# Optimization experiments

Hardware: AMD Instinct MI355X
Metric: run time of the kernel (lower is better)

## Reference

```python
import jax, jax.numpy as jnp
import numpy as np

B, T, D, H = 32, 512, 512, 1024


def setup_inputs() -> dict:
    key = jax.random.key(0)
    k1, k2, k3 = jax.random.split(key, 3)
    X = jax.random.normal(k1, (B, T, D), dtype=jnp.float32)
    # TF GRUCell variables: gates/kernel [D+H, 2H], gates/bias [2H] (init 1.0),
    # candidate/kernel [D+H, H], candidate/bias [H] (init 0.0). Use small random
    # values for a non-degenerate numerical baseline.
    gate_kernel = jax.random.normal(k2, (D + H, 2 * H), dtype=jnp.float32) * 0.02
    gate_bias = jnp.ones((2 * H,), dtype=jnp.float32)
    cand_kernel = jax.random.normal(k3, (D + H, H), dtype=jnp.float32) * 0.02
    cand_bias = jnp.zeros((H,), dtype=jnp.float32)
    return {"X": X, "gate_kernel": gate_kernel, "gate_bias": gate_bias,
            "cand_kernel": cand_kernel, "cand_bias": cand_bias}


def reference(X, gate_kernel, gate_bias, cand_kernel, cand_bias):
    """Static unidirectional GRU (TF GRUCell math), activation=tanh.
    Returns stacked per-step hidden states [B, T, H]; final state is out[:, -1]."""
    h0 = jnp.zeros((X.shape[0], cand_kernel.shape[1]), dtype=X.dtype)

    def step(h, x_t):
        # gates: r (reset), u (update) = sigmoid([x, h] @ Wg + bg)
        gates = jax.nn.sigmoid(jnp.concatenate([x_t, h], axis=-1) @ gate_kernel + gate_bias)
        r, u = jnp.split(gates, 2, axis=-1)
        # candidate: tanh([x, r*h] @ Wc + bc)
        c = jnp.tanh(jnp.concatenate([x_t, r * h], axis=-1) @ cand_kernel + cand_bias)
        h_new = u * h + (1.0 - u) * c
        return h_new, h_new

    _, hs = jax.lax.scan(step, h0, jnp.swapaxes(X, 0, 1))  # hs: [T, B, H]
    return jnp.swapaxes(hs, 0, 1)  # [B, T, H]
```

## Files before the change

kernel.cpp:

```cpp
#include <hip/hip_runtime.h>
#include <hip/hip_bf16.h>

typedef short s8v __attribute__((ext_vector_type(8)));
typedef float f4v __attribute__((ext_vector_type(4)));
typedef unsigned int u4v __attribute__((ext_vector_type(4)));
typedef unsigned int u2v __attribute__((ext_vector_type(2)));

#define NBLK 64
#define TPB 512

constexpr int BB = 32, TT = 512, DD = 512, HH = 1024;
constexpr int KK = DD + HH;
constexpr int PK = KK + 8;
constexpr int PK8 = PK / 8;
constexpr int K8 = KK / 8;

constexpr size_t OFF_WGT = 0;
constexpr size_t SZ_WGT  = (size_t)2 * HH * KK * 2;
constexpr size_t OFF_WCT = OFF_WGT + SZ_WGT;
constexpr size_t SZ_WCT  = (size_t)HH * KK * 2;
constexpr size_t OFF_XBF = OFF_WCT + SZ_WCT;
constexpr size_t SZ_XBF  = (size_t)BB * TT * DD * 2;
constexpr size_t OFF_HPB = OFF_XBF + SZ_XBF;
constexpr size_t SZ_PUB  = (size_t)BB * HH * 2;
constexpr size_t OFF_RPB = OFF_HPB + SZ_PUB;
constexpr size_t OFF_FLG = OFF_RPB + SZ_PUB;
constexpr size_t SZ_FLG  = (size_t)2 * NBLK * 2 * 16 * 4;

__global__ void wtr_kernel(const float* __restrict__ in, unsigned short* __restrict__ out, int N) {
    __shared__ float tl[32][33];
    int tx = threadIdx.x & 31, ty = threadIdx.x >> 5;
    int n0 = blockIdx.x * 32, k0 = blockIdx.y * 32;
#pragma unroll
    for (int r = ty; r < 32; r += 8) tl[r][tx] = in[(size_t)(k0 + r) * N + n0 + tx];
    __syncthreads();
#pragma unroll
    for (int r = ty; r < 32; r += 8) {
        __hip_bfloat16 h = __float2bfloat16(tl[tx][r]);
        out[(size_t)(n0 + r) * KK + k0 + tx] = *reinterpret_cast<unsigned short*>(&h);
    }
}

__global__ void xconv_kernel(const float* __restrict__ X, unsigned short* __restrict__ Xbf) {
    size_t i = ((size_t)blockIdx.x * 256 + threadIdx.x) * 4;
    float4 v = *reinterpret_cast<const float4*>(X + i);
    __hip_bfloat16 h0 = __float2bfloat16(v.x), h1 = __float2bfloat16(v.y);
    __hip_bfloat16 h2 = __float2bfloat16(v.z), h3 = __float2bfloat16(v.w);
    ushort4 o;
    o.x = *(unsigned short*)&h0; o.y = *(unsigned short*)&h1;
    o.z = *(unsigned short*)&h2; o.w = *(unsigned short*)&h3;
    *reinterpret_cast<ushort4*>(Xbf + i) = o;
}

__device__ __forceinline__ u4v cload16(const void* p) {
    u4v r; asm volatile("global_load_dwordx4 %0, %1, off sc0 sc1" : "=v"(r) : "v"(p) : "memory"); return r;
}
__device__ __forceinline__ void cstore8(void* p, u2v v) {
    asm volatile("global_store_dwordx2 %0, %1, off sc0 sc1" :: "v"(p), "v"(v) : "memory");
}
#define B16(x) __builtin_bit_cast(s8v, (x))
#define WAIT_VM(n) do { asm volatile("s_waitcnt vmcnt(" #n ")" ::: "memory"); \
                        __builtin_amdgcn_sched_barrier(0); } while (0)

__device__ __forceinline__ void poll16(const int* f, int blk0, int rtw, int gen, int lane) {
    if (lane < 16) {
        const int* fp = f + ((size_t)(blk0 + lane) * 2 + rtw) * 16;
        while (__hip_atomic_load(fp, __ATOMIC_RELAXED, __HIP_MEMORY_SCOPE_AGENT) < gen)
            __builtin_amdgcn_s_sleep(1);
    }
    asm volatile("" ::: "memory");
}

#define MFMA(A, B, C) __builtin_amdgcn_mfma_f32_16x16x32_bf16((A), (B), (C), 0, 0, 0)

__global__ __launch_bounds__(TPB, 1) void gru_kernel(
    const unsigned short* __restrict__ Xbf,
    const unsigned short* __restrict__ WgT,
    const unsigned short* __restrict__ WcT,
    const float* __restrict__ bg,
    const float* __restrict__ bc,
    float* __restrict__ out,
    unsigned short* __restrict__ hpub,
    unsigned short* __restrict__ rpub,
    int* __restrict__ gflagA,
    int* __restrict__ gflagB)
{
    __shared__ unsigned short sWg[32 * PK];
    __shared__ unsigned short sWc[16 * PK];
    __shared__ float sP[3][2][2][16][16];
    __shared__ unsigned short sStage[32][16];

    const int b    = blockIdx.x;
    const int tid  = threadIdx.x;
    const int wid  = tid >> 6;
    const int lane = tid & 63;
    const int l15  = lane & 15;
    const int lq   = lane >> 4;
    const int ks   = wid >> 1;
    const int rt   = wid & 1;
    const int roff = rt * 16;
    const int arow = roff + l15;
    const int bcol0= b * 16;

    {
        s8v* dst = (s8v*)sWg;
        for (int idx = tid; idx < 32 * K8; idx += TPB) {
            int c = idx / K8, k8 = idx % K8;
            int gc = (c < 16) ? (bcol0 + c) : (HH + bcol0 + (c - 16));
            dst[c * PK8 + k8] = ((const s8v*)(WgT + (size_t)gc * KK))[k8];
        }
        s8v* dst2 = (s8v*)sWc;
        for (int idx = tid; idx < 16 * K8; idx += TPB) {
            int c = idx / K8, k8 = idx % K8;
            dst2[c * PK8 + k8] = ((const s8v*)(WcT + (size_t)(bcol0 + c) * KK))[k8];
        }
    }

    const float bgr = bg[bcol0 + l15];
    const float bgu = bg[HH + bcol0 + l15];
    const float bcv = bc[bcol0 + l15];
    const int   ccol = bcol0 + l15;

    const s8v* sWg8 = (const s8v*)sWg;
    const s8v* sWc8 = (const s8v*)sWc;
    const s8v* bwr = sWg8 + l15 * PK8 + lq;
    const s8v* bwu = sWg8 + (16 + l15) * PK8 + lq;
    const s8v* bwc = sWc8 + l15 * PK8 + lq;
    const s8v* bwrx = bwr + 16 * ks;
    const s8v* bwux = bwu + 16 * ks;
    const s8v* bwrh = bwr + 64 + 32 * ks;
    const s8v* bwuh = bwu + 64 + 32 * ks;
    const s8v* bwcx = bwc + 16 * ks;
    const s8v* bwch = bwc + 64 + 32 * ks;

    float hprev[4] = {0.f, 0.f, 0.f, 0.f};
    float ureg[4]  = {0.f, 0.f, 0.f, 0.f};

    __syncthreads();

#pragma unroll 1
    for (int t = 0; t < TT; ++t) {
        const s8v* xk = (const s8v*)(Xbf + (size_t)arow * (TT * DD) + (size_t)t * DD) + lq + 16 * ks;

        f4v ar0 = {0,0,0,0}, ar1 = {0,0,0,0}, au0 = {0,0,0,0}, au1 = {0,0,0,0};
        {
            s8v x0 = xk[0], x1 = xk[4], x2 = xk[8], x3 = xk[12];
            ar0 = MFMA(x0, bwrx[0],  ar0); au0 = MFMA(x0, bwux[0],  au0);
            ar1 = MFMA(x1, bwrx[4],  ar1); au1 = MFMA(x1, bwux[4],  au1);
            ar0 = MFMA(x2, bwrx[8],  ar0); au0 = MFMA(x2, bwux[8],  au0);
            ar1 = MFMA(x3, bwrx[12], ar1); au1 = MFMA(x3, bwux[12], au1);
        }

        if (t > 0) {
            poll16(gflagB, ks * 16, rt, t, lane);
            const unsigned short* hp = hpub + (size_t)arow * HH + ks * 256 + lq * 8;
            u4v hb[8];
#pragma unroll
            for (int j = 0; j < 8; ++j) hb[j] = cload16(hp + (size_t)j * 32);
            WAIT_VM(4);
            ar0 = MFMA(B16(hb[0]), bwrh[0],  ar0); au0 = MFMA(B16(hb[0]), bwuh[0],  au0);
            ar1 = MFMA(B16(hb[1]), bwrh[4],  ar1); au1 = MFMA(B16(hb[1]), bwuh[4],  au1);
            ar0 = MFMA(B16(hb[2]), bwrh[8],  ar0); au0 = MFMA(B16(hb[2]), bwuh[8],  au0);
            ar1 = MFMA(B16(hb[3]), bwrh[12], ar1); au1 = MFMA(B16(hb[3]), bwuh[12], au1);
            WAIT_VM(0);
            ar0 = MFMA(B16(hb[4]), bwrh[16], ar0); au0 = MFMA(B16(hb[4]), bwuh[16], au0);
            ar1 = MFMA(B16(hb[5]), bwrh[20], ar1); au1 = MFMA(B16(hb[5]), bwuh[20], au1);
            ar0 = MFMA(B16(hb[6]), bwrh[24], ar0); au0 = MFMA(B16(hb[6]), bwuh[24], au0);
            ar1 = MFMA(B16(hb[7]), bwrh[28], ar1); au1 = MFMA(B16(hb[7]), bwuh[28], au1);
        }

        f4v pr = ar0 + ar1, pu = au0 + au1;
        if (ks > 0) {
#pragma unroll
            for (int i = 0; i < 4; ++i) {
                sP[ks - 1][rt][0][lq * 4 + i][l15] = pr[i];
                sP[ks - 1][rt][1][lq * 4 + i][l15] = pu[i];
            }
        }
        __syncthreads();
        float zr[4], zu[4];
        if (ks == 0) {
#pragma unroll
            for (int i = 0; i < 4; ++i) {
                int rr = lq * 4 + i;
                zr[i] = pr[i] + sP[0][rt][0][rr][l15] + sP[1][rt][0][rr][l15]
                              + sP[2][rt][0][rr][l15] + bgr;
                zu[i] = pu[i] + sP[0][rt][1][rr][l15] + sP[1][rt][1][rr][l15]
                              + sP[2][rt][1][rr][l15] + bgu;
            }
        }
        __syncthreads();
        if (ks == 0) {
#pragma unroll
            for (int i = 0; i < 4; ++i) {
                float r = 1.f / (1.f + __expf(-zr[i]));
                ureg[i] = 1.f / (1.f + __expf(-zu[i]));
                __hip_bfloat16 hb16 = __float2bfloat16(r * hprev[i]);
                sStage[roff + lq * 4 + i][l15] = *(unsigned short*)&hb16;
            }
            if (t > 0) {
                int prow = roff + (lane >> 2), pc4 = (lane & 3) * 4;
                u2v v = *reinterpret_cast<const u2v*>(&sStage[prow][pc4]);
                cstore8(rpub + (size_t)prow * HH + bcol0 + pc4, v);
                asm volatile("s_waitcnt vmcnt(0)" ::: "memory");
                if (lane == 0)
                    __hip_atomic_store(&gflagA[(b * 2 + rt) * 16], t,
                                       __ATOMIC_RELAXED, __HIP_MEMORY_SCOPE_AGENT);
            }
        }

        f4v c0 = {0,0,0,0}, c1 = {0,0,0,0};
        {
            s8v x0 = xk[0], x1 = xk[4], x2 = xk[8], x3 = xk[12];
            c0 = MFMA(x0, bwcx[0],  c0); c1 = MFMA(x1, bwcx[4],  c1);
            c0 = MFMA(x2, bwcx[8],  c0); c1 = MFMA(x3, bwcx[12], c1);
        }

        if (t > 0) {
            poll16(gflagA, ks * 16, rt, t, lane);
            const unsigned short* rp = rpub + (size_t)arow * HH + ks * 256 + lq * 8;
            u4v rb[8];
#pragma unroll
            for (int j = 0; j < 8; ++j) rb[j] = cload16(rp + (size_t)j * 32);
            WAIT_VM(4);
            c0 = MFMA(B16(rb[0]), bwch[0],  c0); c1 = MFMA(B16(rb[1]), bwch[4],  c1);
            c0 = MFMA(B16(rb[2]), bwch[8],  c0); c1 = MFMA(B16(rb[3]), bwch[12], c1);
            WAIT_VM(0);
            c0 = MFMA(B16(rb[4]), bwch[16], c0); c1 = MFMA(B16(rb[5]), bwch[20], c1);
            c0 = MFMA(B16(rb[6]), bwch[24], c0); c1 = MFMA(B16(rb[7]), bwch[28], c1);
        }

        f4v pc = c0 + c1;
        if (ks > 0) {
#pragma unroll
            for (int i = 0; i < 4; ++i) sP[ks - 1][rt][0][lq * 4 + i][l15] = pc[i];
        }
        __syncthreads();
        float zc[4];
        if (ks == 0) {
#pragma unroll
            for (int i = 0; i < 4; ++i) {
                int rr = lq * 4 + i;
                zc[i] = pc[i] + sP[0][rt][0][rr][l15] + sP[1][rt][0][rr][l15]
                              + sP[2][rt][0][rr][l15] + bcv;
            }
        }
        __syncthreads();
        if (ks == 0) {
#pragma unroll
            for (int i = 0; i < 4; ++i) {
                float e = __expf(2.f * zc[i]);
                float cv = 1.f - 2.f / (e + 1.f);
                float hn = ureg[i] * hprev[i] + (1.f - ureg[i]) * cv;
                hprev[i] = hn;
                __hip_bfloat16 hb16 = __float2bfloat16(hn);
                sStage[roff + lq * 4 + i][l15] = *(unsigned short*)&hb16;
            }
            int prow = roff + (lane >> 2), pc4 = (lane & 3) * 4;
            u2v v = *reinterpret_cast<const u2v*>(&sStage[prow][pc4]);
            cstore8(hpub + (size_t)prow * HH + bcol0 + pc4, v);
            asm volatile("s_waitcnt vmcnt(0)" ::: "memory");
            if (lane == 0)
                __hip_atomic_store(&gflagB[(b * 2 + rt) * 16], t + 1,
                                   __ATOMIC_RELAXED, __HIP_MEMORY_SCOPE_AGENT);
#pragma unroll
            for (int i = 0; i < 4; ++i) {
                int row = roff + lq * 4 + i;
                out[(size_t)row * (TT * HH) + (size_t)t * HH + ccol] = hprev[i];
            }
        }
    }
}

extern "C" void kernel_launch(void* const* d_in, const int* in_sizes, int n_in,
                              void* d_out, int out_size, void* d_ws, size_t ws_size,
                              hipStream_t stream) {
    const float* X  = (const float*)d_in[0];
    const float* gk = (const float*)d_in[1];
    const float* gb = (const float*)d_in[2];
    const float* ck = (const float*)d_in[3];
    const float* cb = (const float*)d_in[4];
    float* out = (float*)d_out;
    char* ws = (char*)d_ws;
    if (ws_size < OFF_FLG + SZ_FLG) return;

    unsigned short* WgT  = (unsigned short*)(ws + OFF_WGT);
    unsigned short* WcT  = (unsigned short*)(ws + OFF_WCT);
    unsigned short* Xbf  = (unsigned short*)(ws + OFF_XBF);
    unsigned short* hpub = (unsigned short*)(ws + OFF_HPB);
    unsigned short* rpub = (unsigned short*)(ws + OFF_RPB);
    int*            gflagA = (int*)(ws + OFF_FLG);
    int*            gflagB = gflagA + NBLK * 2 * 16;

    hipMemsetAsync(gflagA, 0, SZ_FLG, stream);

    dim3 tb(256);
    wtr_kernel<<<dim3(2 * HH / 32, KK / 32), tb, 0, stream>>>(gk, WgT, 2 * HH);
    wtr_kernel<<<dim3(HH / 32, KK / 32), tb, 0, stream>>>(ck, WcT, HH);
    xconv_kernel<<<(BB * TT * DD) / (256 * 4), tb, 0, stream>>>(X, Xbf);

    gru_kernel<<<NBLK, dim3(TPB), 0, stream>>>(Xbf, WgT, WcT, gb, cb, out,
                                               hpub, rpub, gflagA, gflagB);
}
```

Baseline: 3.914 ms.

## Embed step-tag in bf16 exponent bits to validate data without flag polling

Published h and r*h values are scaled by a per-step power of two so that their bf16 exponent bits carry a step class tag. Consumers load the data speculatively, check the tag bits, and fall back to flag polling only when the data is stale. The r buffer is double-buffered, the store-then-flag wait is removed, and the x-part MFMAs are overlapped with the speculative loads. This is meant to cut the cross-block handshake latency on each step, at the cost of clamping tiny magnitudes, relying on value-range assumptions that could break correctness, and retry loops when reads arrive early.

```diff
diff --git a/kernel.cpp b/kernel.cpp
--- a/kernel.cpp
+++ b/kernel.cpp
@@ -14,6 +14,7 @@
 constexpr int PK = KK + 8;
 constexpr int PK8 = PK / 8;
 constexpr int K8 = KK / 8;
+constexpr size_t BBHH = (size_t)BB * HH;
 
 constexpr size_t OFF_WGT = 0;
 constexpr size_t SZ_WGT  = (size_t)2 * HH * KK * 2;
@@ -22,9 +23,9 @@
 constexpr size_t OFF_XBF = OFF_WCT + SZ_WCT;
 constexpr size_t SZ_XBF  = (size_t)BB * TT * DD * 2;
 constexpr size_t OFF_HPB = OFF_XBF + SZ_XBF;
-constexpr size_t SZ_PUB  = (size_t)BB * HH * 2;
+constexpr size_t SZ_PUB  = BBHH * 2;
 constexpr size_t OFF_RPB = OFF_HPB + SZ_PUB;
-constexpr size_t OFF_FLG = OFF_RPB + SZ_PUB;
+constexpr size_t OFF_FLG = OFF_RPB + 2 * SZ_PUB;
 constexpr size_t SZ_FLG  = (size_t)2 * NBLK * 2 * 16 * 4;
 
 __global__ void wtr_kernel(const float* __restrict__ in, unsigned short* __restrict__ out, int N) {
@@ -58,6 +59,9 @@
 __device__ __forceinline__ void cstore8(void* p, u2v v) {
     asm volatile("global_store_dwordx2 %0, %1, off sc0 sc1" :: "v"(p), "v"(v) : "memory");
 }
+__device__ __forceinline__ void cstore4(void* p, int v) {
+    asm volatile("global_store_dword %0, %1, off sc0 sc1" :: "v"(p), "v"(v) : "memory");
+}
 #define B16(x) __builtin_bit_cast(s8v, (x))
 #define WAIT_VM(n) do { asm volatile("s_waitcnt vmcnt(" #n ")" ::: "memory"); \
                         __builtin_amdgcn_sched_barrier(0); } while (0)
@@ -72,6 +76,26 @@
 }
 
 #define MFMA(A, B, C) __builtin_amdgcn_mfma_f32_16x16x32_bf16((A), (B), (C), 0, 0, 0)
+
+__device__ __forceinline__ float enc(float h, float s) {
+    float a = __builtin_fmaxf(__builtin_fabsf(h), 9.313225746154785e-10f);
+    return __builtin_copysignf(a, h) * s;
+}
+__device__ __forceinline__ float cls_scale(int c) {
+    return __builtin_bit_cast(float, (unsigned)(127 + 32 * c) << 23);
+}
+__device__ __forceinline__ float cls_inv(int c) {
+    return __builtin_bit_cast(float, (unsigned)(127 - 32 * c) << 23);
+}
+__device__ __forceinline__ unsigned cls_pat(int c) {
+    return 0x30003000u + (unsigned)c * 0x10001000u;
+}
+#define VALID8(arr, e, bad) do { bad = 0u; \
+    _Pragma("unroll") for (int j_ = 0; j_ < 8; ++j_) { \
+        bad |= ((arr)[j_][0] & 0x70007000u) ^ (e); \
+        bad |= ((arr)[j_][1] & 0x70007000u) ^ (e); \
+        bad |= ((arr)[j_][2] & 0x70007000u) ^ (e); \
+        bad |= ((arr)[j_][3] & 0x70007000u) ^ (e); } } while (0)
 
 __global__ __launch_bounds__(TPB, 1) void gru_kernel(
     const unsigned short* __restrict__ Xbf,
@@ -88,7 +112,7 @@
     __shared__ unsigned short sWg[32 * PK];
     __shared__ unsigned short sWc[16 * PK];
     __shared__ float sP[3][2][2][16][16];
-    __shared__ unsigned short sStage[32][16];
+    __shared__ unsigned short sStage[2][16][16];
 
     const int b    = blockIdx.x;
     const int tid  = threadIdx.x;
@@ -116,9 +140,9 @@
         }
     }
 
-    const float bgr = bg[bcol0 + l15];
-    const float bgu = bg[HH + bcol0 + l15];
-    const float bcv = bc[bcol0 + l15];
+    const float bgr  = bg[bcol0 + l15];
+    const float bgu  = bg[HH + bcol0 + l15];
+    const float bcv  = bc[bcol0 + l15];
     const int   ccol = bcol0 + l15;
 
     const s8v* sWg8 = (const s8v*)sWg;
@@ -141,35 +165,47 @@
 #pragma unroll 1
     for (int t = 0; t < TT; ++t) {
         const s8v* xk = (const s8v*)(Xbf + (size_t)arow * (TT * DD) + (size_t)t * DD) + lq + 16 * ks;
-
-        f4v ar0 = {0,0,0,0}, ar1 = {0,0,0,0}, au0 = {0,0,0,0}, au1 = {0,0,0,0};
-        {
-            s8v x0 = xk[0], x1 = xk[4], x2 = xk[8], x3 = xk[12];
-            ar0 = MFMA(x0, bwrx[0],  ar0); au0 = MFMA(x0, bwux[0],  au0);
-            ar1 = MFMA(x1, bwrx[4],  ar1); au1 = MFMA(x1, bwux[4],  au1);
-            ar0 = MFMA(x2, bwrx[8],  ar0); au0 = MFMA(x2, bwux[8],  au0);
-            ar1 = MFMA(x3, bwrx[12], ar1); au1 = MFMA(x3, bwux[12], au1);
-        }
-
+        s8v x0 = xk[0], x1 = xk[4], x2 = xk[8], x3 = xk[12];
+
+        u4v hb[8];
+        const unsigned short* hp = hpub + (size_t)arow * HH + ks * 256 + lq * 8;
         if (t > 0) {
-            poll16(gflagB, ks * 16, rt, t, lane);
-            const unsigned short* hp = hpub + (size_t)arow * HH + ks * 256 + lq * 8;
-            u4v hb[8];
 #pragma unroll
             for (int j = 0; j < 8; ++j) hb[j] = cload16(hp + (size_t)j * 32);
-            WAIT_VM(4);
-            ar0 = MFMA(B16(hb[0]), bwrh[0],  ar0); au0 = MFMA(B16(hb[0]), bwuh[0],  au0);
-            ar1 = MFMA(B16(hb[1]), bwrh[4],  ar1); au1 = MFMA(B16(hb[1]), bwuh[4],  au1);
-            ar0 = MFMA(B16(hb[2]), bwrh[8],  ar0); au0 = MFMA(B16(hb[2]), bwuh[8],  au0);
-            ar1 = MFMA(B16(hb[3]), bwrh[12], ar1); au1 = MFMA(B16(hb[3]), bwuh[12], au1);
+        }
+        f4v axr = {0,0,0,0}, axu = {0,0,0,0};
+        axr = MFMA(x0, bwrx[0],  axr); axu = MFMA(x0, bwux[0],  axu);
+        axr = MFMA(x1, bwrx[4],  axr); axu = MFMA(x1, bwux[4],  axu);
+        axr = MFMA(x2, bwrx[8],  axr); axu = MFMA(x2, bwux[8],  axu);
+        axr = MFMA(x3, bwrx[12], axr); axu = MFMA(x3, bwux[12], axu);
+
+        f4v ahr0 = {0,0,0,0}, ahr1 = {0,0,0,0}, ahu0 = {0,0,0,0}, ahu1 = {0,0,0,0};
+        if (t > 0) {
             WAIT_VM(0);
-            ar0 = MFMA(B16(hb[4]), bwrh[16], ar0); au0 = MFMA(B16(hb[4]), bwuh[16], au0);
-            ar1 = MFMA(B16(hb[5]), bwrh[20], ar1); au1 = MFMA(B16(hb[5]), bwuh[20], au1);
-            ar0 = MFMA(B16(hb[6]), bwrh[24], ar0); au0 = MFMA(B16(hb[6]), bwuh[24], au0);
-            ar1 = MFMA(B16(hb[7]), bwrh[28], ar1); au1 = MFMA(B16(hb[7]), bwuh[28], au1);
-        }
-
-        f4v pr = ar0 + ar1, pu = au0 + au1;
+            const unsigned eA = cls_pat((t - 1) & 3);
+            unsigned bad; VALID8(hb, eA, bad);
+            if (__any(bad != 0)) {
+                poll16(gflagB, ks * 16, rt, t, lane);
+                do {
+#pragma unroll
+                    for (int j = 0; j < 8; ++j) hb[j] = cload16(hp + (size_t)j * 32);
+                    WAIT_VM(0);
+                    VALID8(hb, eA, bad);
+                } while (__any(bad != 0));
+            }
+            ahr0 = MFMA(B16(hb[0]), bwrh[0],  ahr0); ahu0 = MFMA(B16(hb[0]), bwuh[0],  ahu0);
+            ahr1 = MFMA(B16(hb[1]), bwrh[4],  ahr1); ahu1 = MFMA(B16(hb[1]), bwuh[4],  ahu1);
+            ahr0 = MFMA(B16(hb[2]), bwrh[8],  ahr0); ahu0 = MFMA(B16(hb[2]), bwuh[8],  ahu0);
+            ahr1 = MFMA(B16(hb[3]), bwrh[12], ahr1); ahu1 = MFMA(B16(hb[3]), bwuh[12], ahu1);
+            ahr0 = MFMA(B16(hb[4]), bwrh[16], ahr0); ahu0 = MFMA(B16(hb[4]), bwuh[16], ahu0);
+            ahr1 = MFMA(B16(hb[5]), bwrh[20], ahr1); ahu1 = MFMA(B16(hb[5]), bwuh[20], ahu1);
+            ahr0 = MFMA(B16(hb[6]), bwrh[24], ahr0); ahu0 = MFMA(B16(hb[6]), bwuh[24], ahu0);
+            ahr1 = MFMA(B16(hb[7]), bwrh[28], ahr1); ahu1 = MFMA(B16(hb[7]), bwuh[28], ahu1);
+        }
+        const float hinv = cls_inv((t - 1) & 3);
+        f4v pr = axr + (ahr0 + ahr1) * hinv;
+        f4v pu = axu + (ahu0 + ahu1) * hinv;
+
         if (ks > 0) {
 #pragma unroll
             for (int i = 0; i < 4; ++i) {
@@ -190,47 +226,56 @@
             }
         }
         __syncthreads();
+        const float sEnc = cls_scale(t & 3);
         if (ks == 0) {
 #pragma unroll
             for (int i = 0; i < 4; ++i) {
                 float r = 1.f / (1.f + __expf(-zr[i]));
                 ureg[i] = 1.f / (1.f + __expf(-zu[i]));
-                __hip_bfloat16 hb16 = __float2bfloat16(r * hprev[i]);
-                sStage[roff + lq * 4 + i][l15] = *(unsigned short*)&hb16;
+                __hip_bfloat16 hb16 = __float2bfloat16(enc(r * hprev[i], sEnc));
+                sStage[rt][lq * 4 + i][l15] = *(unsigned short*)&hb16;
             }
             if (t > 0) {
-                int prow = roff + (lane >> 2), pc4 = (lane & 3) * 4;
-                u2v v = *reinterpret_cast<const u2v*>(&sStage[prow][pc4]);
-                cstore8(rpub + (size_t)prow * HH + bcol0 + pc4, v);
-                asm volatile("s_waitcnt vmcnt(0)" ::: "memory");
-                if (lane == 0)
-                    __hip_atomic_store(&gflagA[(b * 2 + rt) * 16], t,
-                                       __ATOMIC_RELAXED, __HIP_MEMORY_SCOPE_AGENT);
-            }
-        }
-
-        f4v c0 = {0,0,0,0}, c1 = {0,0,0,0};
-        {
-            s8v x0 = xk[0], x1 = xk[4], x2 = xk[8], x3 = xk[12];
-            c0 = MFMA(x0, bwcx[0],  c0); c1 = MFMA(x1, bwcx[4],  c1);
-            c0 = MFMA(x2, bwcx[8],  c0); c1 = MFMA(x3, bwcx[12], c1);
-        }
-
+                int prow = lane >> 2, pc4 = (lane & 3) * 4;
+                u2v v = *reinterpret_cast<const u2v*>(&sStage[rt][prow][pc4]);
+                cstore8(rpub + (size_t)(t & 1) * BBHH + (size_t)(roff + prow) * HH + bcol0 + pc4, v);
+                if (lane == 0) cstore4(gflagA + (b * 2 + rt) * 16, t);
+            }
+        }
+
+        u4v rb[8];
+        const unsigned short* rp = rpub + (size_t)(t & 1) * BBHH
+                                 + (size_t)arow * HH + ks * 256 + lq * 8;
         if (t > 0) {
-            poll16(gflagA, ks * 16, rt, t, lane);
-            const unsigned short* rp = rpub + (size_t)arow * HH + ks * 256 + lq * 8;
-            u4v rb[8];
 #pragma unroll
             for (int j = 0; j < 8; ++j) rb[j] = cload16(rp + (size_t)j * 32);
-            WAIT_VM(4);
-            c0 = MFMA(B16(rb[0]), bwch[0],  c0); c1 = MFMA(B16(rb[1]), bwch[4],  c1);
-            c0 = MFMA(B16(rb[2]), bwch[8],  c0); c1 = MFMA(B16(rb[3]), bwch[12], c1);
+        }
+        f4v cx0 = {0,0,0,0}, cx1 = {0,0,0,0};
+        cx0 = MFMA(x0, bwcx[0],  cx0); cx1 = MFMA(x1, bwcx[4],  cx1);
+        cx0 = MFMA(x2, bwcx[8],  cx0); cx1 = MFMA(x3, bwcx[12], cx1);
+
+        f4v ch0 = {0,0,0,0}, ch1 = {0,0,0,0};
+        if (t > 0) {
             WAIT_VM(0);
-            c0 = MFMA(B16(rb[4]), bwch[16], c0); c1 = MFMA(B16(rb[5]), bwch[20], c1);
-            c0 = MFMA(B16(rb[6]), bwch[24], c0); c1 = MFMA(B16(rb[7]), bwch[28], c1);
-        }
-
-        f4v pc = c0 + c1;
+            const unsigned eB = cls_pat(t & 3);
+            unsigned bad; VALID8(rb, eB, bad);
+            if (__any(bad != 0)) {
+                poll16(gflagA, ks * 16, rt, t, lane);
+                do {
+#pragma unroll
+                    for (int j = 0; j < 8; ++j) rb[j] = cload16(rp + (size_t)j * 32);
+                    WAIT_VM(0);
+                    VALID8(rb, eB, bad);
+                } while (__any(bad != 0));
+            }
+            ch0 = MFMA(B16(rb[0]), bwch[0],  ch0); ch1 = MFMA(B16(rb[1]), bwch[4],  ch1);
+            ch0 = MFMA(B16(rb[2]), bwch[8],  ch0); ch1 = MFMA(B16(rb[3]), bwch[12], ch1);
+            ch0 = MFMA(B16(rb[4]), bwch[16], ch0); ch1 = MFMA(B16(rb[5]), bwch[20], ch1);
+            ch0 = MFMA(B16(rb[6]), bwch[24], ch0); ch1 = MFMA(B16(rb[7]), bwch[28], ch1);
+        }
+        const float rinv = cls_inv(t & 3);
+        f4v pc = (cx0 + cx1) + (ch0 + ch1) * rinv;
+
         if (ks > 0) {
 #pragma unroll
             for (int i = 0; i < 4; ++i) sP[ks - 1][rt][0][lq * 4 + i][l15] = pc[i];
@@ -253,16 +298,13 @@
                 float cv = 1.f - 2.f / (e + 1.f);
                 float hn = ureg[i] * hprev[i] + (1.f - ureg[i]) * cv;
                 hprev[i] = hn;
-                __hip_bfloat16 hb16 = __float2bfloat16(hn);
-                sStage[roff + lq * 4 + i][l15] = *(unsigned short*)&hb16;
-            }
-            int prow = roff + (lane >> 2), pc4 = (lane & 3) * 4;
-            u2v v = *reinterpret_cast<const u2v*>(&sStage[prow][pc4]);
-            cstore8(hpub + (size_t)prow * HH + bcol0 + pc4, v);
-            asm volatile("s_waitcnt vmcnt(0)" ::: "memory");
-            if (lane == 0)
-                __hip_atomic_store(&gflagB[(b * 2 + rt) * 16], t + 1,
-                                   __ATOMIC_RELAXED, __HIP_MEMORY_SCOPE_AGENT);
+                __hip_bfloat16 hb16 = __float2bfloat16(enc(hn, sEnc));
+                sStage[rt][lq * 4 + i][l15] = *(unsigned short*)&hb16;
+            }
+            int prow = lane >> 2, pc4 = (lane & 3) * 4;
+            u2v v = *reinterpret_cast<const u2v*>(&sStage[rt][prow][pc4]);
+            cstore8(hpub + (size_t)(roff + prow) * HH + bcol0 + pc4, v);
+            if (lane == 0) cstore4(gflagB + (b * 2 + rt) * 16, t + 1);
 #pragma unroll
             for (int i = 0; i < 4; ++i) {
                 int row = roff + lq * 4 + i;
@@ -292,6 +334,7 @@
     int*            gflagA = (int*)(ws + OFF_FLG);
     int*            gflagB = gflagA + NBLK * 2 * 16;
 
+    hipMemsetAsync(hpub, 0x7F, 3 * SZ_PUB, stream);
     hipMemsetAsync(gflagA, 0, SZ_FLG, stream);
 
     dim3 tb(256);
```

New measurement: 5.565 ms. 1.42x slower.
